# Performance work log

Hardware: AMD Instinct MI355X
Metric: run time of the kernel (lower is better)

Reference implementation:

```python
import math
import jax, jax.numpy as jnp
import numpy as np

B, S, D, H = 4, 2048, 1024, 16
DK = D // H
THETA = 10000.0


def _rope(xh, pos):
    # xh: [B, H, S, DK], pos: [S]
    half = jnp.arange(0, DK, 2, dtype=jnp.float32) / DK
    inv_freq = THETA ** (-half)                      # [DK/2]
    ang = pos.astype(jnp.float32)[:, None] * inv_freq  # [S, DK/2]
    cos, sin = jnp.cos(ang).astype(xh.dtype), jnp.sin(ang).astype(xh.dtype)
    x1, x2 = xh[..., 0::2], xh[..., 1::2]
    r1 = x1 * cos - x2 * sin
    r2 = x1 * sin + x2 * cos
    return jnp.stack([r1, r2], axis=-1).reshape(xh.shape)


def setup_inputs() -> dict:
    key = jax.random.key(0)
    kx, kq, kk, kv, ko = jax.random.split(key, 5)
    std = 0.02
    x = jax.random.normal(kx, (B, S, D), jnp.float32)
    wq = jax.random.normal(kq, (D, D), jnp.float32) * std
    wk = jax.random.normal(kk, (D, D), jnp.float32) * std
    wv = jax.random.normal(kv, (D, D), jnp.float32) * std
    wo = jax.random.normal(ko, (D, D), jnp.float32) * std
    token_positions = jnp.arange(S, dtype=jnp.int32)
    return {"x": x, "wq": wq, "wk": wk, "wv": wv, "wo": wo,
            "token_positions": token_positions}


def reference(x, wq, wk, wv, wo, token_positions):
    # bias-free linear projections: y = x @ W^T (torch Linear convention)
    q = x @ wq.T
    k = x @ wk.T
    v = x @ wv.T
    # split heads: [B, S, D] -> [B, H, S, DK]
    to_heads = lambda t: t.reshape(B, S, H, DK).transpose(0, 2, 1, 3)
    qh, kh, vh = to_heads(q), to_heads(k), to_heads(v)
    qh = _rope(qh, token_positions)
    kh = _rope(kh, token_positions)
    scores = jnp.einsum('bhqd,bhkd->bhqk', qh, kh) / math.sqrt(DK)
    causal = jnp.tril(jnp.ones((S, S), dtype=bool))
    scores = jnp.where(causal, scores, -jnp.inf)
    attn = jax.nn.softmax(scores, axis=-1)
    out = jnp.einsum('bhqk,bhkd->bhqd', attn, vh)       # [B, H, S, DK]
    out = out.transpose(0, 2, 1, 3).reshape(B, S, D)    # merge heads
    return out @ wo.T
```

## Files before the change

### kernel.cpp

```cpp
#include <hip/hip_runtime.h>

#define B_ 4
#define S_ 2048
#define D_ 1024
#define H_ 16
#define DK_ 64
#define M_ (B_*S_)
#define K_ D_
#define N_ D_

typedef unsigned short u16;
typedef unsigned int u32;
typedef __bf16 bf16x8 __attribute__((ext_vector_type(8)));
typedef float f32x4 __attribute__((ext_vector_type(4)));
typedef u32 u32x4v __attribute__((ext_vector_type(4)));

#define EXP2F(x) __builtin_amdgcn_exp2f(x)

__device__ __forceinline__ u16 f2bf(float f) {
    u32 u = __builtin_bit_cast(u32, f);
    u += 0x7fff + ((u >> 16) & 1);
    return (u16)(u >> 16);
}
__device__ __forceinline__ float bf2f(u16 h) {
    u32 u = ((u32)h) << 16;
    return __builtin_bit_cast(float, u);
}
__device__ __forceinline__ u32 pack_trunc(float a, float b) {
    return (__builtin_bit_cast(u32, a) >> 16) | (__builtin_bit_cast(u32, b) & 0xffff0000u);
}

#define GLDS16(g, l) __builtin_amdgcn_global_load_lds( \
    (__attribute__((address_space(1))) void*)(g),      \
    (__attribute__((address_space(3))) void*)(l), 16, 0, 0)

__global__ __launch_bounds__(256) void cvt_x(const float* __restrict__ in,
                                             u16* __restrict__ out, int n4) {
    const int i = blockIdx.x * 256 + threadIdx.x;
    if (i >= n4) return;
    const float4 f = *(const float4*)(in + (size_t)i * 4);
    u32 p0 = (u32)f2bf(f.x) | ((u32)f2bf(f.y) << 16);
    u32 p1 = (u32)f2bf(f.z) | ((u32)f2bf(f.w) << 16);
    *(uint2*)(out + (size_t)i * 4) = make_uint2(p0, p1);
}

__global__ __launch_bounds__(256) void cvt_w4(
    const float* __restrict__ w0, const float* __restrict__ w1,
    const float* __restrict__ w2, const float* __restrict__ w3,
    u16* __restrict__ o0, u16* __restrict__ o1,
    u16* __restrict__ o2, u16* __restrict__ o3) {
    const int wi = blockIdx.y;
    const float* in = (wi == 0) ? w0 : (wi == 1) ? w1 : (wi == 2) ? w2 : w3;
    u16* out       = (wi == 0) ? o0 : (wi == 1) ? o1 : (wi == 2) ? o2 : o3;
    const int i = blockIdx.x * 256 + threadIdx.x;
    const float4 f = *(const float4*)(in + (size_t)i * 4);
    u32 p0 = (u32)f2bf(f.x) | ((u32)f2bf(f.y) << 16);
    u32 p1 = (u32)f2bf(f.z) | ((u32)f2bf(f.w) << 16);
    *(uint2*)(out + (size_t)i * 4) = make_uint2(p0, p1);
}

template <int MODE>
__device__ __forceinline__ void gemm_tile(const u16* __restrict__ A,
                                          const u16* __restrict__ Bm,
                                          void* __restrict__ Cv,
                                          int m0, int n0) {
    __shared__ u16 As[2][128 * 32];
    __shared__ u16 Bs[2][128 * 32];
    const int tid  = threadIdx.x;
    const int wave = tid >> 6, lane = tid & 63;
    const int wm = wave & 1, wn = wave >> 1;
    const int quad = lane >> 4, mcol = lane & 15;

    const int c0 = wave, c1 = wave + 4;
    const int r0 = c0 * 16 + (lane >> 2), r1 = c1 * 16 + (lane >> 2);
    const int kb = (((lane & 3) ^ ((lane >> 3) & 3)) * 8);
    const u16* ga0 = A  + (size_t)(m0 + r0) * K_ + kb;
    const u16* ga1 = A  + (size_t)(m0 + r1) * K_ + kb;
    const u16* gb0 = Bm + (size_t)(n0 + r0) * K_ + kb;
    const u16* gb1 = Bm + (size_t)(n0 + r1) * K_ + kb;
    const int lo0 = c0 * 512, lo1 = c1 * 512;
    const int rsw = ((mcol >> 1) & 3);

    f32x4 acc[4][4];
#pragma unroll
    for (int i = 0; i < 4; i++)
#pragma unroll
        for (int j = 0; j < 4; j++) acc[i][j] = f32x4{0.f, 0.f, 0.f, 0.f};

    GLDS16(ga0, &As[0][lo0]); GLDS16(ga1, &As[0][lo1]);
    GLDS16(gb0, &Bs[0][lo0]); GLDS16(gb1, &Bs[0][lo1]);
    ga0 += 32; ga1 += 32; gb0 += 32; gb1 += 32;
    __syncthreads();

    for (int kt = 0; kt < K_; kt += 32) {
        const int cur = (kt >> 5) & 1;
        if (kt + 32 < K_) {
            const int nxt = cur ^ 1;
            GLDS16(ga0, &As[nxt][lo0]); GLDS16(ga1, &As[nxt][lo1]);
            GLDS16(gb0, &Bs[nxt][lo0]); GLDS16(gb1, &Bs[nxt][lo1]);
            ga0 += 32; ga1 += 32; gb0 += 32; gb1 += 32;
        }

        bf16x8 af[4], bfr[4];
#pragma unroll
        for (int i = 0; i < 4; i++) {
            af[i]  = *(const bf16x8*)&As[cur][(wm * 64 + i * 16 + mcol) * 32 + ((quad ^ rsw)) * 8];
            bfr[i] = *(const bf16x8*)&Bs[cur][(wn * 64 + i * 16 + mcol) * 32 + ((quad ^ rsw)) * 8];
        }
#pragma unroll
        for (int i = 0; i < 4; i++)
#pragma unroll
            for (int j = 0; j < 4; j++)
                acc[i][j] = __builtin_amdgcn_mfma_f32_16x16x32_bf16(
                    af[i], bfr[j], acc[i][j], 0, 0, 0);

        __syncthreads();
    }

#pragma unroll
    for (int i = 0; i < 4; i++) {
        const int row = m0 + wm * 64 + i * 16 + quad * 4;
#pragma unroll
        for (int j = 0; j < 4; j++) {
            const int col = n0 + wn * 64 + j * 16 + mcol;
            if constexpr (MODE == 2) {
                const int hh = col >> 6, dd = col & 63;
                const int bb = row >> 11, ss = row & 2047;
                const u32 lo = (u32)f2bf(acc[i][j][0]) | ((u32)f2bf(acc[i][j][1]) << 16);
                const u32 hi = (u32)f2bf(acc[i][j][2]) | ((u32)f2bf(acc[i][j][3]) << 16);
                *(uint2*)((u16*)Cv + ((size_t)((bb * H_ + hh) * DK_ + dd)) * S_ + ss) =
                    make_uint2(lo, hi);
            } else {
#pragma unroll
                for (int r = 0; r < 4; r++) {
                    if constexpr (MODE == 1)
                        ((float*)Cv)[(size_t)(row + r) * N_ + col] = acc[i][j][r];
                    else
                        ((u16*)Cv)[(size_t)(row + r) * N_ + col] = f2bf(acc[i][j][r]);
                }
            }
        }
    }
}

__global__ __launch_bounds__(256) void gemm_qkv_kernel(
    const u16* __restrict__ x,
    const u16* __restrict__ wq, const u16* __restrict__ wk,
    const u16* __restrict__ wv,
    u16* __restrict__ q, u16* __restrict__ k, u16* __restrict__ vt) {
    const int flat = blockIdx.x;
    const int w = (flat & 7) * 192 + (flat >> 3);
    const int my = w / 24;
    const int rem = w - my * 24;
    const int z = rem >> 3, nx = rem & 7;
    const int m0 = my * 128, n0 = nx * 128;
    if (z == 2) {
        gemm_tile<2>(x, wv, vt, m0, n0);
    } else {
        const u16* Bm = z ? wk : wq;
        u16* C        = z ? k  : q;
        gemm_tile<0>(x, Bm, C, m0, n0);
    }
}

__global__ __launch_bounds__(256) void gemm_out_kernel(
    const u16* __restrict__ o, const u16* __restrict__ wo, float* __restrict__ out) {
    const int flat = blockIdx.x;
    const int w = (flat & 7) * 64 + (flat >> 3);
    const int my = w >> 3, nx = w & 7;
    gemm_tile<1>(o, wo, out, my * 128, nx * 128);
}

__global__ __launch_bounds__(256) void rope_qk(u16* __restrict__ q,
                                               u16* __restrict__ k,
                                               const int* __restrict__ pos) {
    const int idx = blockIdx.x * 256 + threadIdx.x;
    const int seg = idx & 3;
    const int h = (idx >> 2) & (H_ - 1);
    const int s = (idx >> 6) & (S_ - 1);
    const int b = idx >> 17;
    const float p = (float)pos[s];
    const float QSC = 0.18033688011112042f;
    const size_t off = ((size_t)(b * S_ + s)) * D_ + h * DK_ + seg * 16;

    u32 qa[8], ka[8];
    *(uint4*)&qa[0] = *(const uint4*)(q + off);
    *(uint4*)&qa[4] = *(const uint4*)(q + off + 8);
    *(uint4*)&ka[0] = *(const uint4*)(k + off);
    *(uint4*)&ka[4] = *(const uint4*)(k + off + 8);
#pragma unroll
    for (int w = 0; w < 8; w++) {
        const int i = seg * 8 + w;
        const float inv = exp2f((float)i * (-13.287712379549449f / 32.f));
        const float ang = p * inv;
        float sn, cs;
        __sincosf(ang, &sn, &cs);
        {
            const float x1 = bf2f((u16)(qa[w] & 0xffff));
            const float x2 = bf2f((u16)(qa[w] >> 16));
            qa[w] = (u32)f2bf((x1 * cs - x2 * sn) * QSC) |
                    ((u32)f2bf((x1 * sn + x2 * cs) * QSC) << 16);
        }
        {
            const float x1 = bf2f((u16)(ka[w] & 0xffff));
            const float x2 = bf2f((u16)(ka[w] >> 16));
            ka[w] = (u32)f2bf(x1 * cs - x2 * sn) |
                    ((u32)f2bf(x1 * sn + x2 * cs) << 16);
        }
    }
    *(uint4*)(q + off)     = *(uint4*)&qa[0];
    *(uint4*)(q + off + 8) = *(uint4*)&qa[4];
    *(uint4*)(k + off)     = *(uint4*)&ka[0];
    *(uint4*)(k + off + 8) = *(uint4*)&ka[4];
}

__global__ __launch_bounds__(256) void attn_kernel(
    const u16* __restrict__ q, const u16* __restrict__ k,
    const u16* __restrict__ vt, u16* __restrict__ o) {
    __shared__ u16 Ks[64 * 64];
    __shared__ u16 Vs[64 * 64];

    const int tid = threadIdx.x, wave = tid >> 6, lane = tid & 63;
    const int flat = blockIdx.x;
    const int qp = flat >> 6;
    const int h = flat & (H_ - 1);
    const int b = (flat >> 4) & 3;
    const int quad = lane >> 4, mcol = lane & 15;
    const int srd = mcol & 7;

    const int rr2 = tid >> 2, cc2 = tid & 3;
    const int sw = rr2 & 7;
    const int so0 = rr2 * 64 + (((cc2 * 2)     ^ sw) << 3);
    const int so1 = rr2 * 64 + (((cc2 * 2 + 1) ^ sw) << 3);
    const int prr = (rr2 & 35) | ((rr2 & 12) << 1) | ((rr2 & 16) >> 2);
    const int ch2 = cc2 * 16;
    const u16* krow = k + ((size_t)(b * S_ + prr)) * D_ + h * DK_ + ch2;
    const u16* vrow = vt + ((size_t)((b * H_ + h) * DK_ + rr2)) * S_ + ch2;

    u32x4v onesw;
    onesw[0] = onesw[1] = onesw[2] = onesw[3] = 0x3F803F80u;
    const bf16x8 onesf = __builtin_bit_cast(bf16x8, onesw);

    for (int pass = 0; pass < 2; pass++) {
        const int qt = pass ? (15 - qp) : qp;
        const int q0 = qt * 128;
        const int wq0 = q0 + wave * 32;
        const int jmax = 2 * qt + 1;

        bf16x8 qf[2][2];
#pragma unroll
        for (int g = 0; g < 2; g++) {
            const u16* qs = q + ((size_t)(b * S_ + wq0 + g * 16 + mcol)) * D_ + h * DK_ + quad * 8;
            qf[g][0] = *(const bf16x8*)qs;
            qf[g][1] = *(const bf16x8*)(qs + 32);
        }

        float m[2] = {-1e30f, -1e30f};
        f32x4 lacc[2];
        f32x4 oacc[2][4];
#pragma unroll
        for (int g = 0; g < 2; g++) {
            lacc[g] = f32x4{0.f, 0.f, 0.f, 0.f};
#pragma unroll
            for (int dn = 0; dn < 4; dn++) oacc[g][dn] = f32x4{0.f, 0.f, 0.f, 0.f};
        }

        uint4 kr0 = *(const uint4*)(krow);
        uint4 kr1 = *(const uint4*)(krow + 8);
        uint4 vr0 = *(const uint4*)(vrow);
        uint4 vr1 = *(const uint4*)(vrow + 8);

        for (int j = 0; j <= jmax; j++) {
            __syncthreads();
            *(uint4*)&Ks[so0] = kr0;
            *(uint4*)&Ks[so1] = kr1;
            *(uint4*)&Vs[so0] = vr0;
            *(uint4*)&Vs[so1] = vr1;
            __syncthreads();

            if (j < jmax) {
                kr0 = *(const uint4*)(krow + (size_t)(j + 1) * 64 * D_);
                kr1 = *(const uint4*)(krow + (size_t)(j + 1) * 64 * D_ + 8);
                vr0 = *(const uint4*)(vrow + (j + 1) * 64);
                vr1 = *(const uint4*)(vrow + (j + 1) * 64 + 8);
            }

            if (j * 64 > wq0 + 31) continue;

            f32x4 st[2][4];
            __builtin_amdgcn_s_setprio(1);
#pragma unroll
            for (int n = 0; n < 4; n++) {
                const u16* kl = &Ks[(n * 16 + mcol) * 64];
                bf16x8 kf0 = *(const bf16x8*)&kl[(quad ^ srd) << 3];
                bf16x8 kf1 = *(const bf16x8*)&kl[((quad | 4) ^ srd) << 3];
                f32x4 z0 = f32x4{0.f, 0.f, 0.f, 0.f};
                z0 = __builtin_amdgcn_mfma_f32_16x16x32_bf16(kf0, qf[0][0], z0, 0, 0, 0);
                z0 = __builtin_amdgcn_mfma_f32_16x16x32_bf16(kf1, qf[0][1], z0, 0, 0, 0);
                st[0][n] = z0;
                f32x4 z1 = f32x4{0.f, 0.f, 0.f, 0.f};
                z1 = __builtin_amdgcn_mfma_f32_16x16x32_bf16(kf0, qf[1][0], z1, 0, 0, 0);
                z1 = __builtin_amdgcn_mfma_f32_16x16x32_bf16(kf1, qf[1][1], z1, 0, 0, 0);
                st[1][n] = z1;
            }
            __builtin_amdgcn_s_setprio(0);

            if (j * 64 + 63 > wq0) {
#pragma unroll
                for (int g = 0; g < 2; g++) {
                    const int qg = wq0 + g * 16 + mcol;
#pragma unroll
                    for (int n = 0; n < 4; n++) {
                        const int tb = j * 64 + ((n >> 1) << 5) + ((n & 1) << 2) + quad * 8;
#pragma unroll
                        for (int r = 0; r < 4; r++)
                            if (tb + r > qg) st[g][n][r] = -1e30f;
                    }
                }
            }

#pragma unroll
            for (int g = 0; g < 2; g++) {
                float mx = st[g][0][0];
#pragma unroll
                for (int n = 0; n < 4; n++)
#pragma unroll
                    for (int r = 0; r < 4; r++) mx = fmaxf(mx, st[g][n][r]);
                mx = fmaxf(mx, __shfl_xor(mx, 16));
                mx = fmaxf(mx, __shfl_xor(mx, 32));
                const bool need = !__all(mx <= m[g] + 8.f);
                if (need) {
                    const float mnew = fmaxf(m[g], mx);
                    const float al = EXP2F(m[g] - mnew);
                    m[g] = mnew;
                    float alphaT[4];
#pragma unroll
                    for (int r = 0; r < 4; r++) alphaT[r] = __shfl(al, quad * 4 + r);
#pragma unroll
                    for (int dn = 0; dn < 4; dn++)
#pragma unroll
                        for (int r = 0; r < 4; r++) oacc[g][dn][r] *= alphaT[r];
#pragma unroll
                    for (int r = 0; r < 4; r++) lacc[g][r] *= alphaT[r];
                }
#pragma unroll
                for (int n = 0; n < 4; n++)
#pragma unroll
                    for (int r = 0; r < 4; r++)
                        st[g][n][r] = EXP2F(st[g][n][r] - m[g]);
            }

            bf16x8 pf[2][2];
#pragma unroll
            for (int g = 0; g < 2; g++) {
                u32x4v w0, w1;
                w0[0] = pack_trunc(st[g][0][0], st[g][0][1]);
                w0[1] = pack_trunc(st[g][0][2], st[g][0][3]);
                w0[2] = pack_trunc(st[g][1][0], st[g][1][1]);
                w0[3] = pack_trunc(st[g][1][2], st[g][1][3]);
                w1[0] = pack_trunc(st[g][2][0], st[g][2][1]);
                w1[1] = pack_trunc(st[g][2][2], st[g][2][3]);
                w1[2] = pack_trunc(st[g][3][0], st[g][3][1]);
                w1[3] = pack_trunc(st[g][3][2], st[g][3][3]);
                pf[g][0] = __builtin_bit_cast(bf16x8, w0);
                pf[g][1] = __builtin_bit_cast(bf16x8, w1);
            }

            __builtin_amdgcn_s_setprio(1);
#pragma unroll
            for (int g = 0; g < 2; g++) {
                lacc[g] = __builtin_amdgcn_mfma_f32_16x16x32_bf16(pf[g][0], onesf, lacc[g], 0, 0, 0);
                lacc[g] = __builtin_amdgcn_mfma_f32_16x16x32_bf16(pf[g][1], onesf, lacc[g], 0, 0, 0);
            }
#pragma unroll
            for (int dn = 0; dn < 4; dn++) {
                const u16* vl = &Vs[(dn * 16 + mcol) * 64];
                bf16x8 vf0 = *(const bf16x8*)&vl[(quad ^ srd) << 3];
                bf16x8 vf1 = *(const bf16x8*)&vl[((quad | 4) ^ srd) << 3];
#pragma unroll
                for (int g = 0; g < 2; g++) {
                    oacc[g][dn] = __builtin_amdgcn_mfma_f32_16x16x32_bf16(pf[g][0], vf0, oacc[g][dn], 0, 0, 0);
                    oacc[g][dn] = __builtin_amdgcn_mfma_f32_16x16x32_bf16(pf[g][1], vf1, oacc[g][dn], 0, 0, 0);
                }
            }
            __builtin_amdgcn_s_setprio(0);
        }

#pragma unroll
        for (int g = 0; g < 2; g++) {
            float linv[4];
#pragma unroll
            for (int r = 0; r < 4; r++) linv[r] = 1.f / lacc[g][r];
#pragma unroll
            for (int dn = 0; dn < 4; dn++)
#pragma unroll
                for (int r = 0; r < 4; r++) {
                    const int row = wq0 + g * 16 + quad * 4 + r;
                    o[((size_t)(b * S_ + row)) * D_ + h * DK_ + dn * 16 + mcol] =
                        f2bf(oacc[g][dn][r] * linv[r]);
                }
        }
    }
}

extern "C" void kernel_launch(void* const* d_in, const int* in_sizes, int n_in,
                              void* d_out, int out_size, void* d_ws, size_t ws_size,
                              hipStream_t stream) {
    const float* x  = (const float*)d_in[0];
    const float* wq = (const float*)d_in[1];
    const float* wk = (const float*)d_in[2];
    const float* wv = (const float*)d_in[3];
    const float* wo = (const float*)d_in[4];
    const int*   tp = (const int*)d_in[5];
    float* out = (float*)d_out;

    u16* ws = (u16*)d_ws;
    const size_t NE = (size_t)M_ * D_;
    const size_t WE = (size_t)N_ * K_;
    u16* xb  = ws;
    u16* wqb = ws + NE;
    u16* wkb = wqb + WE;
    u16* wvb = wkb + WE;
    u16* wob = wvb + WE;
    u16* qb  = wob + WE;
    u16* kb  = qb + NE;
    u16* vtb = (u16*)d_out;
    u16* ob  = xb;

    dim3 blk(256);
    cvt_x<<<dim3((int)(NE / 1024)), blk, 0, stream>>>(x, xb, (int)(NE / 4));
    cvt_w4<<<dim3((int)(WE / 1024), 4), blk, 0, stream>>>(wq, wk, wv, wo, wqb, wkb, wvb, wob);

    gemm_qkv_kernel<<<dim3(3 * (M_ / 128) * (N_ / 128)), blk, 0, stream>>>(xb, wqb, wkb, wvb, qb, kb, vtb);
    rope_qk<<<dim3((B_ * S_ * H_ * 4) / 256), blk, 0, stream>>>(qb, kb, tp);
    attn_kernel<<<dim3((S_ / 128 / 2) * H_ * B_), blk, 0, stream>>>(qb, kb, vtb, ob);
    gemm_out_kernel<<<dim3((M_ / 128) * (N_ / 128)), blk, 0, stream>>>(ob, wob, out);
}
```

Baseline: 255.4 us.

## Triple-buffer GEMM LDS tiles with explicit vmcnt waits and one barrier

The projection GEMM tile loop moves from double buffering to a three-stage LDS ring, prefetching two k-steps ahead. The syncthreads calls are replaced by explicit s_waitcnt vmcnt/lgkmcnt waits and a single s_barrier per step, and the MFMA block is raised with s_setprio. The aim is to hide global-to-LDS load latency and remove one barrier per iteration. The cost is 50% more LDS per block, which may lower occupancy, and the hand-counted vmcnt values must match the number of outstanding loads.

```diff
diff --git a/kernel.cpp b/kernel.cpp
--- a/kernel.cpp
+++ b/kernel.cpp
@@ -8,6 +8,7 @@
 #define M_ (B_*S_)
 #define K_ D_
 #define N_ D_
+#define NSTEP 32
 
 typedef unsigned short u16;
 typedef unsigned int u32;
@@ -63,9 +64,9 @@
 __device__ __forceinline__ void gemm_tile(const u16* __restrict__ A,
                                           const u16* __restrict__ Bm,
                                           void* __restrict__ Cv,
-                                          int m0, int n0) {
-    __shared__ u16 As[2][128 * 32];
-    __shared__ u16 Bs[2][128 * 32];
+                                          int m0, int n0,
+                                          u16* __restrict__ As,
+                                          u16* __restrict__ Bs) {
     const int tid  = threadIdx.x;
     const int wave = tid >> 6, lane = tid & 63;
     const int wm = wave & 1, wn = wave >> 1;
@@ -87,34 +88,47 @@
 #pragma unroll
         for (int j = 0; j < 4; j++) acc[i][j] = f32x4{0.f, 0.f, 0.f, 0.f};
 
-    GLDS16(ga0, &As[0][lo0]); GLDS16(ga1, &As[0][lo1]);
-    GLDS16(gb0, &Bs[0][lo0]); GLDS16(gb1, &Bs[0][lo1]);
+    GLDS16(ga0, As + lo0); GLDS16(ga1, As + lo1);
+    GLDS16(gb0, Bs + lo0); GLDS16(gb1, Bs + lo1);
     ga0 += 32; ga1 += 32; gb0 += 32; gb1 += 32;
-    __syncthreads();
-
-    for (int kt = 0; kt < K_; kt += 32) {
-        const int cur = (kt >> 5) & 1;
-        if (kt + 32 < K_) {
-            const int nxt = cur ^ 1;
-            GLDS16(ga0, &As[nxt][lo0]); GLDS16(ga1, &As[nxt][lo1]);
-            GLDS16(gb0, &Bs[nxt][lo0]); GLDS16(gb1, &Bs[nxt][lo1]);
+    GLDS16(ga0, As + 4096 + lo0); GLDS16(ga1, As + 4096 + lo1);
+    GLDS16(gb0, Bs + 4096 + lo0); GLDS16(gb1, Bs + 4096 + lo1);
+    ga0 += 32; ga1 += 32; gb0 += 32; gb1 += 32;
+
+    int cur = 0, tgt = 2;
+    for (int t = 0; t < NSTEP; ++t) {
+        if (t < NSTEP - 1) asm volatile("s_waitcnt vmcnt(4)" ::: "memory");
+        else               asm volatile("s_waitcnt vmcnt(0)" ::: "memory");
+        asm volatile("s_waitcnt lgkmcnt(0)" ::: "memory");
+        __builtin_amdgcn_s_barrier();
+
+        if (t < NSTEP - 2) {
+            u16* at = As + tgt * 4096;
+            u16* bt = Bs + tgt * 4096;
+            GLDS16(ga0, at + lo0); GLDS16(ga1, at + lo1);
+            GLDS16(gb0, bt + lo0); GLDS16(gb1, bt + lo1);
             ga0 += 32; ga1 += 32; gb0 += 32; gb1 += 32;
         }
 
+        const u16* Ab = As + cur * 4096;
+        const u16* Bb = Bs + cur * 4096;
         bf16x8 af[4], bfr[4];
 #pragma unroll
         for (int i = 0; i < 4; i++) {
-            af[i]  = *(const bf16x8*)&As[cur][(wm * 64 + i * 16 + mcol) * 32 + ((quad ^ rsw)) * 8];
-            bfr[i] = *(const bf16x8*)&Bs[cur][(wn * 64 + i * 16 + mcol) * 32 + ((quad ^ rsw)) * 8];
-        }
+            af[i]  = *(const bf16x8*)&Ab[(wm * 64 + i * 16 + mcol) * 32 + (quad ^ rsw) * 8];
+            bfr[i] = *(const bf16x8*)&Bb[(wn * 64 + i * 16 + mcol) * 32 + (quad ^ rsw) * 8];
+        }
+        __builtin_amdgcn_s_setprio(1);
 #pragma unroll
         for (int i = 0; i < 4; i++)
 #pragma unroll
             for (int j = 0; j < 4; j++)
                 acc[i][j] = __builtin_amdgcn_mfma_f32_16x16x32_bf16(
                     af[i], bfr[j], acc[i][j], 0, 0, 0);
-
-        __syncthreads();
+        __builtin_amdgcn_s_setprio(0);
+
+        cur = (cur == 2) ? 0 : cur + 1;
+        tgt = (tgt == 2) ? 0 : tgt + 1;
     }
 
 #pragma unroll
@@ -148,6 +162,8 @@
     const u16* __restrict__ wq, const u16* __restrict__ wk,
     const u16* __restrict__ wv,
     u16* __restrict__ q, u16* __restrict__ k, u16* __restrict__ vt) {
+    __shared__ u16 As[3 * 4096];
+    __shared__ u16 Bs[3 * 4096];
     const int flat = blockIdx.x;
     const int w = (flat & 7) * 192 + (flat >> 3);
     const int my = w / 24;
@@ -155,20 +171,22 @@
     const int z = rem >> 3, nx = rem & 7;
     const int m0 = my * 128, n0 = nx * 128;
     if (z == 2) {
-        gemm_tile<2>(x, wv, vt, m0, n0);
+        gemm_tile<2>(x, wv, vt, m0, n0, As, Bs);
     } else {
         const u16* Bm = z ? wk : wq;
         u16* C        = z ? k  : q;
-        gemm_tile<0>(x, Bm, C, m0, n0);
+        gemm_tile<0>(x, Bm, C, m0, n0, As, Bs);
     }
 }
 
 __global__ __launch_bounds__(256) void gemm_out_kernel(
     const u16* __restrict__ o, const u16* __restrict__ wo, float* __restrict__ out) {
+    __shared__ u16 As[3 * 4096];
+    __shared__ u16 Bs[3 * 4096];
     const int flat = blockIdx.x;
     const int w = (flat & 7) * 64 + (flat >> 3);
     const int my = w >> 3, nx = w & 7;
-    gemm_tile<1>(o, wo, out, my * 128, nx * 128);
+    gemm_tile<1>(o, wo, out, my * 128, nx * 128, As, Bs);
 }
 
 __global__ __launch_bounds__(256) void rope_qk(u16* __restrict__ q,
```

After: 260.5 us. 1.02x slower.
